# Kernel tuning notes

Hardware: AMD Instinct MI355X
Metric: run time of the kernel (lower is better)

The kernel has to match this reference:

```python
import jax, jax.numpy as jnp
import numpy as np

KERNEL = 3          # kernel_size = (3, 3)
DEGREE = 3          # spline_order -> Chebyshev polynomial degree
N_CONVS = 8


def setup_inputs() -> dict:
    key = jax.random.key(0)
    k1, k2, k3, k4 = jax.random.split(key, 4)
    x = jax.random.normal(k1, (16, 16, 128, 128), jnp.float32)
    # per-conv learned params of ChebyshevKANLinear(in=9, out=1), stacked over n_convs
    cheby_coeffs = jax.random.normal(k2, (N_CONVS, KERNEL * KERNEL, DEGREE + 1), jnp.float32) * 0.1
    base_weight = jax.random.normal(k3, (N_CONVS, KERNEL * KERNEL), jnp.float32) * (1.0 / 3.0)
    spline_scaler = 1.0 + 0.1 * jax.random.normal(k4, (N_CONVS, KERNEL * KERNEL), jnp.float32)
    return {"x": x, "cheby_coeffs": cheby_coeffs,
            "base_weight": base_weight, "spline_scaler": spline_scaler}


def _kan_conv2d(x, cheby_coeffs, base_weight, spline_scaler):
    # x: (B, C, H, W); each channel unfolded independently (as torch Unfold per-channel),
    # each of N_CONVS KAN kernels applied to every channel -> out channels C*N_CONVS.
    B, C, H, W = x.shape
    patches = jax.lax.conv_general_dilated_patches(
        x, (KERNEL, KERNEL), (1, 1), [(1, 1), (1, 1)])  # (B, C*9, Ho, Wo), channel-major
    Ho, Wo = patches.shape[-2], patches.shape[-1]
    p = patches.reshape(B, C, KERNEL * KERNEL, Ho * Wo)
    p = jnp.moveaxis(p, 2, 3)  # (B, C, P, 9) where P = Ho*Wo patches

    # base (skip) path: SiLU(x) @ base_weight^T
    base = jnp.einsum('bcpi,ji->bcjp', jax.nn.silu(p), base_weight)

    # spline path: Chebyshev basis on tanh-normalized input
    t = jnp.tanh(p)
    Ts = [jnp.ones_like(t), t]
    for _ in range(DEGREE - 1):
        Ts.append(2.0 * t * Ts[-1] - Ts[-2])
    Tb = jnp.stack(Ts, axis=-1)  # (B, C, P, 9, DEGREE+1)
    w = cheby_coeffs * spline_scaler[..., None]  # (n_convs, 9, D+1)
    spline = jnp.einsum('bcpik,jik->bcjp', Tb, w)

    out = (base + spline).reshape(B, C * N_CONVS, Ho, Wo)
    return out


def reference(x, cheby_coeffs, base_weight, spline_scaler):
    return _kan_conv2d(x, cheby_coeffs, base_weight, spline_scaler)
```

## Files before the change

kernel.cpp:

```cpp
#include <hip/hip_runtime.h>

#define BATCH 16
#define CH    16
#define HH    128
#define WW    128
#define NC    8
#define TR    8
#define BPB   4
#define HR    (TR + 2)
#define FW    (WW + 2)
#define NELEM (HR * FW)
#define NSTG  ((NELEM + 255) / 256)

#define CFENCE asm volatile("" ::: "memory")

__global__ __launch_bounds__(256, 4)
void kan_conv_kernel(const float* __restrict__ x,
                     const float* __restrict__ cheby,
                     const float* __restrict__ bwt,
                     const float* __restrict__ scl,
                     float* __restrict__ out)
{
    __shared__ float4 feat[HR][FW];
    __shared__ float4 wgt[9 * NC];
    __shared__ float  bias[NC];

    const int tid   = threadIdx.x;
    const int bz    = blockIdx.y;
    const int band0 = blockIdx.x * (TR * BPB);

    const float* xp = x + (size_t)bz * HH * WW;

    if (tid < 9 * NC) {
        int j = tid / 9, i = tid % 9;
        float s = scl[j * 9 + i];
        wgt[i * NC + j] = make_float4(bwt[j * 9 + i],
                                      cheby[(j * 9 + i) * 4 + 1] * s,
                                      cheby[(j * 9 + i) * 4 + 2] * s,
                                      cheby[(j * 9 + i) * 4 + 3] * s);
    } else if (tid >= 128 && tid < 128 + NC) {
        int j = tid - 128;
        float b = 0.f;
        #pragma unroll
        for (int i = 0; i < 9; ++i)
            b += (cheby[(j * 9 + i) * 4 + 0] - cheby[(j * 9 + i) * 4 + 2]) * scl[j * 9 + i];
        bias[j] = b;
    }

    float v[NSTG];
    #pragma unroll
    for (int k = 0; k < NSTG; ++k) {
        int idx = tid + 256 * k;
        int row = idx / FW;
        int col = idx - row * FW;
        int gh  = band0 + row - 1;
        int gw  = col - 1;
        float nv = 0.f;
        if (idx < NELEM && (unsigned)gh < (unsigned)HH && (unsigned)gw < (unsigned)WW)
            nv = xp[gh * WW + gw];
        v[k] = nv;
    }

    for (int bb = 0; bb < BPB; ++bb) {
        const int band = band0 + bb * TR;

        if (bb) { CFENCE; __builtin_amdgcn_s_barrier(); CFENCE; }

        #pragma unroll
        for (int k = 0; k < NSTG; ++k) {
            int idx = tid + 256 * k;
            if (idx < NELEM) {
                int row = idx / FW;
                int col = idx - row * FW;
                float val = v[k];
                float e1 = __expf(val);
                float e2 = e1 * e1;
                float sg = 1.f - __builtin_amdgcn_rcpf(1.f + e1);
                float t  = 1.f - 2.f * __builtin_amdgcn_rcpf(e2 + 1.f);
                float f2 = 2.f * t * t;
                float f3 = 2.f * t * (f2 - 1.f) - t;
                feat[row][col] = make_float4(val * sg, t, f2, f3);
            }
        }

        asm volatile("s_waitcnt lgkmcnt(0)" ::: "memory");
        __builtin_amdgcn_s_barrier();
        CFENCE;

        if (bb + 1 < BPB) {
            const int nb = band + TR;
            #pragma unroll
            for (int k = 0; k < NSTG; ++k) {
                int idx = tid + 256 * k;
                int row = idx / FW;
                int col = idx - row * FW;
                int gh  = nb + row - 1;
                int gw  = col - 1;
                float nv = 0.f;
                if (idx < NELEM && (unsigned)gh < (unsigned)HH && (unsigned)gw < (unsigned)WW)
                    nv = xp[gh * WW + gw];
                v[k] = nv;
            }
        }

        const int c  = tid & 127;
        const int r0 = tid >> 7;

        float acc[4][NC];
        #pragma unroll
        for (int s = 0; s < 4; ++s)
            #pragma unroll
            for (int j = 0; j < NC; ++j)
                acc[s][j] = bias[j];

        #pragma unroll
        for (int dr = 0; dr < 3; ++dr) {
            #pragma unroll
            for (int dc = 0; dc < 3; ++dc) {
                float4 f[4];
                #pragma unroll
                for (int s = 0; s < 4; ++s)
                    f[s] = feat[r0 + 2 * s + dr][c + dc];
                #pragma unroll
                for (int j = 0; j < NC; ++j) {
                    float4 w = wgt[(dr * 3 + dc) * NC + j];
                    #pragma unroll
                    for (int s = 0; s < 4; ++s) {
                        acc[s][j] += w.x * f[s].x;
                        acc[s][j] += w.y * f[s].y;
                        acc[s][j] += w.z * f[s].z;
                        acc[s][j] += w.w * f[s].w;
                    }
                }
            }
        }

        float* op = out + (size_t)(bz * NC) * HH * WW + (size_t)(band + r0) * WW + c;
        #pragma unroll
        for (int j = 0; j < NC; ++j)
            #pragma unroll
            for (int s = 0; s < 4; ++s)
                op[(size_t)j * HH * WW + s * 2 * WW] = acc[s][j];
    }
}

extern "C" void kernel_launch(void* const* d_in, const int* in_sizes, int n_in,
                              void* d_out, int out_size, void* d_ws, size_t ws_size,
                              hipStream_t stream) {
    const float* x     = (const float*)d_in[0];
    const float* cheby = (const float*)d_in[1];
    const float* bwt   = (const float*)d_in[2];
    const float* scl   = (const float*)d_in[3];
    float* out = (float*)d_out;

    dim3 grid(HH / (TR * BPB), BATCH * CH);
    dim3 block(256);
    hipLaunchKernelGGL(kan_conv_kernel, grid, block, 0, stream, x, cheby, bwt, scl, out);
}
```

Before: 161.7 us.

## Remap threads so each wave owns two output convs with register row reuse

Reworks the compute mapping: each 64-lane wave handles two of the eight output convs for all 8 rows and two column halves. It loads a full column of feature rows into registers and reuses them across the three vertical taps, and weights are made wave-uniform via readfirstlane so they can live in scalar registers. Bands per block drop from 4 to 2, which doubles the grid, and the hand-written barriers become __syncthreads. This cuts LDS feature reads per FMA but raises register pressure, since 32 accumulators and 10 float4 features are live at once.

```diff
diff --git a/kernel.cpp b/kernel.cpp
--- a/kernel.cpp
+++ b/kernel.cpp
@@ -6,15 +6,14 @@
 #define WW    128
 #define NC    8
 #define TR    8
-#define BPB   4
+#define BPB   2
 #define HR    (TR + 2)
 #define FW    (WW + 2)
 #define NELEM (HR * FW)
-#define NSTG  ((NELEM + 255) / 256)
+#define NTHR  256
+#define NSTG  6
 
-#define CFENCE asm volatile("" ::: "memory")
-
-__global__ __launch_bounds__(256, 4)
+__global__ __launch_bounds__(NTHR, 4)
 void kan_conv_kernel(const float* __restrict__ x,
                      const float* __restrict__ cheby,
                      const float* __restrict__ bwt,
@@ -28,8 +27,8 @@
     const int tid   = threadIdx.x;
     const int bz    = blockIdx.y;
     const int band0 = blockIdx.x * (TR * BPB);
-
-    const float* xp = x + (size_t)bz * HH * WW;
+    const int lane  = tid & 63;
+    const int pp    = tid >> 6;
 
     if (tid < 9 * NC) {
         int j = tid / 9, i = tid % 9;
@@ -47,10 +46,11 @@
         bias[j] = b;
     }
 
+    const float* xp = x + (size_t)bz * HH * WW;
     float v[NSTG];
     #pragma unroll
     for (int k = 0; k < NSTG; ++k) {
-        int idx = tid + 256 * k;
+        int idx = tid + NTHR * k;
         int row = idx / FW;
         int col = idx - row * FW;
         int gh  = band0 + row - 1;
@@ -63,12 +63,11 @@
 
     for (int bb = 0; bb < BPB; ++bb) {
         const int band = band0 + bb * TR;
-
-        if (bb) { CFENCE; __builtin_amdgcn_s_barrier(); CFENCE; }
+        if (bb) __syncthreads();
 
         #pragma unroll
         for (int k = 0; k < NSTG; ++k) {
-            int idx = tid + 256 * k;
+            int idx = tid + NTHR * k;
             if (idx < NELEM) {
                 int row = idx / FW;
                 int col = idx - row * FW;
@@ -82,16 +81,13 @@
                 feat[row][col] = make_float4(val * sg, t, f2, f3);
             }
         }
-
-        asm volatile("s_waitcnt lgkmcnt(0)" ::: "memory");
-        __builtin_amdgcn_s_barrier();
-        CFENCE;
+        __syncthreads();
 
         if (bb + 1 < BPB) {
             const int nb = band + TR;
             #pragma unroll
             for (int k = 0; k < NSTG; ++k) {
-                int idx = tid + 256 * k;
+                int idx = tid + NTHR * k;
                 int row = idx / FW;
                 int col = idx - row * FW;
                 int gh  = nb + row - 1;
@@ -103,44 +99,61 @@
             }
         }
 
-        const int c  = tid & 127;
-        const int r0 = tid >> 7;
-
-        float acc[4][NC];
-        #pragma unroll
-        for (int s = 0; s < 4; ++s)
+        float acc[TR][2][2];
+        {
+            float b0 = bias[pp * 2];
+            float b1 = bias[pp * 2 + 1];
             #pragma unroll
-            for (int j = 0; j < NC; ++j)
-                acc[s][j] = bias[j];
+            for (int s = 0; s < TR; ++s)
+                #pragma unroll
+                for (int h = 0; h < 2; ++h) {
+                    acc[s][h][0] = b0;
+                    acc[s][h][1] = b1;
+                }
+        }
 
         #pragma unroll
-        for (int dr = 0; dr < 3; ++dr) {
+        for (int dc = 0; dc < 3; ++dc) {
+            float ws[3][2][4];
             #pragma unroll
-            for (int dc = 0; dc < 3; ++dc) {
-                float4 f[4];
+            for (int dr = 0; dr < 3; ++dr)
                 #pragma unroll
-                for (int s = 0; s < 4; ++s)
-                    f[s] = feat[r0 + 2 * s + dr][c + dc];
+                for (int q = 0; q < 2; ++q) {
+                    float4 wv = wgt[(dr * 3 + dc) * NC + pp * 2 + q];
+                    ws[dr][q][0] = __uint_as_float(__builtin_amdgcn_readfirstlane(__float_as_uint(wv.x)));
+                    ws[dr][q][1] = __uint_as_float(__builtin_amdgcn_readfirstlane(__float_as_uint(wv.y)));
+                    ws[dr][q][2] = __uint_as_float(__builtin_amdgcn_readfirstlane(__float_as_uint(wv.z)));
+                    ws[dr][q][3] = __uint_as_float(__builtin_amdgcn_readfirstlane(__float_as_uint(wv.w)));
+                }
+            #pragma unroll
+            for (int h = 0; h < 2; ++h) {
+                float4 f[HR];
                 #pragma unroll
-                for (int j = 0; j < NC; ++j) {
-                    float4 w = wgt[(dr * 3 + dc) * NC + j];
+                for (int r = 0; r < HR; ++r)
+                    f[r] = feat[r][h * 64 + lane + dc];
+                #pragma unroll
+                for (int dr = 0; dr < 3; ++dr)
                     #pragma unroll
-                    for (int s = 0; s < 4; ++s) {
-                        acc[s][j] += w.x * f[s].x;
-                        acc[s][j] += w.y * f[s].y;
-                        acc[s][j] += w.z * f[s].z;
-                        acc[s][j] += w.w * f[s].w;
-                    }
-                }
+                    for (int q = 0; q < 2; ++q)
+                        #pragma unroll
+                        for (int s = 0; s < TR; ++s) {
+                            acc[s][h][q] += ws[dr][q][0] * f[s + dr].x;
+                            acc[s][h][q] += ws[dr][q][1] * f[s + dr].y;
+                            acc[s][h][q] += ws[dr][q][2] * f[s + dr].z;
+                            acc[s][h][q] += ws[dr][q][3] * f[s + dr].w;
+                        }
             }
         }
 
-        float* op = out + (size_t)(bz * NC) * HH * WW + (size_t)(band + r0) * WW + c;
+        float* op = out + (size_t)(bz * NC + pp * 2) * HH * WW
+                        + (size_t)band * WW + lane;
         #pragma unroll
-        for (int j = 0; j < NC; ++j)
+        for (int q = 0; q < 2; ++q)
             #pragma unroll
-            for (int s = 0; s < 4; ++s)
-                op[(size_t)j * HH * WW + s * 2 * WW] = acc[s][j];
+            for (int s = 0; s < TR; ++s)
+                #pragma unroll
+                for (int h = 0; h < 2; ++h)
+                    op[(size_t)q * HH * WW + (size_t)s * WW + h * 64] = acc[s][h][q];
     }
 }
 
@@ -154,6 +167,6 @@
     float* out = (float*)d_out;
 
     dim3 grid(HH / (TR * BPB), BATCH * CH);
-    dim3 block(256);
+    dim3 block(NTHR);
     hipLaunchKernelGGL(kan_conv_kernel, grid, block, 0, stream, x, cheby, bwt, scl, out);
 }
```

Measured after the change: 166.2 us. 1.03x slower.
